# Performance work log

Hardware: AMD Instinct MI355X
Metric: run time of the kernel (lower is better)

## Reference

```python
import jax, jax.numpy as jnp
import numpy as np

DN = ('NCHW', 'OIHW', 'NCHW')

def _conv(x, w, b):
    y = jax.lax.conv_general_dilated(x, w, (2, 2), 'SAME', dimension_numbers=DN)
    return jax.nn.relu(y + b[None, :, None, None])

def setup_inputs() -> dict:
    key = jax.random.key(0)
    ks = jax.random.split(key, 20)
    B, S, V, D, NC = 64, 128, 32000, 512, 1000
    inp = {}
    inp['images'] = jax.random.normal(ks[0], (B, 3, 224, 224), jnp.float32)
    inp['sequences'] = jax.random.randint(ks[1], (B, S), 0, V)
    inp['lengths'] = jax.random.randint(ks[2], (B,), 1, S + 1)
    inp['lengths_var'] = inp['lengths']
    s = 0.02
    inp['emb'] = jax.random.normal(ks[3], (V, D), jnp.float32) * s
    # SimpleCNN(3): 4 strided conv blocks 3->64->128->256->512, final_dim=512
    chans = [3, 64, 128, 256, 512]
    for i in range(4):
        inp[f'cw{i+1}'] = jax.random.normal(ks[4 + i], (chans[i + 1], chans[i], 3, 3), jnp.float32) * s
        inp[f'cb{i+1}'] = jnp.zeros((chans[i + 1],), jnp.float32)
    inp['rnn_w'] = jax.random.normal(ks[8], (D, D), jnp.float32) * s
    inp['rnn_b'] = jnp.zeros((D,), jnp.float32)
    inp['fc1_w'] = jax.random.normal(ks[9], (D + 512, 512), jnp.float32) * s
    inp['fc1_b'] = jnp.zeros((512,), jnp.float32)
    inp['fc2_w'] = jax.random.normal(ks[10], (512, 512), jnp.float32) * s
    inp['fc2_b'] = jnp.zeros((512,), jnp.float32)
    inp['clf_w'] = jax.random.normal(ks[11], (512, NC), jnp.float32) * s
    inp['clf_b'] = jnp.zeros((NC,), jnp.float32)
    return inp

def reference(images, sequences, lengths, lengths_var, emb, cw1, cb1, cw2, cb2, cw3, cb3, cw4, cb4, rnn_w, rnn_b, fc1_w, fc1_b, fc2_w, fc2_b, clf_w, clf_b):
    B, S = sequences.shape
    # masked mean over valid tokens (replaces the per-sample python loop)
    we = emb[sequences]                                   # [B,S,512]
    mask = (jnp.arange(S)[None, :] < lengths[:, None]).astype(we.dtype)
    batch_means = (we * mask[:, :, None]).sum(1) / lengths.astype(we.dtype)[:, None]
    sent = batch_means @ rnn_w + rnn_b                    # [B,512]
    # SimpleCNN + global avg pool -> [B,512,1,1] -> squeeze
    x = _conv(images, cw1, cb1)
    x = _conv(x, cw2, cb2)
    x = _conv(x, cw3, cb3)
    x = _conv(x, cw4, cb4)
    img = x.mean(axis=(2, 3))                             # [B,512]
    feats = jnp.concatenate([img, sent], axis=1)          # [B,1024]
    h = jax.nn.relu(feats @ fc1_w + fc1_b)
    h = jax.nn.relu(h @ fc2_w + fc2_b)                    # dropout = identity (eval)
    return h @ clf_w + clf_b
```

## Files before the change

### kernel.cpp

```cpp
#include <hip/hip_runtime.h>
#include <hip/hip_bf16.h>
#include <cstddef>
#include <cstdint>

typedef unsigned short u16;
typedef __attribute__((ext_vector_type(8))) short bf16x8;
typedef __attribute__((ext_vector_type(4))) float f32x4;
typedef __attribute__((ext_vector_type(8))) unsigned short u16x8;

static __device__ __forceinline__ u16 f2bf(float x) {
  unsigned u = __float_as_uint(x);
  u += 0x7fffu + ((u >> 16) & 1u);
  return (u16)(u >> 16);
}
static __device__ __forceinline__ float bflo(unsigned u) { return __uint_as_float(u << 16); }
static __device__ __forceinline__ float bfhi(unsigned u) { return __uint_as_float(u & 0xffff0000u); }

static __device__ __forceinline__ void gll16(const u16* g, u16* l) {
  __builtin_amdgcn_global_load_lds(
      (const __attribute__((address_space(1))) void*)g,
      (__attribute__((address_space(3))) void*)l, 16, 0, 0);
}

static __device__ __forceinline__ int xcd_swizzle(int orig, int nwg) {
  const int q = nwg >> 3, r = nwg & 7;
  const int xcd = orig & 7, idx = orig >> 3;
  return (xcd < r ? xcd * (q + 1) : r * (q + 1) + (xcd - r) * q) + idx;
}


static __device__ __forceinline__ void halo_store_f(u16* buf, int IH, int PC,
                                                    int C, long long i) {
  const int c8n = C >> 3;
  const int c8 = (int)(i % c8n);
  long long rem = i / c8n;
  const int per = 2 * PC + 2 * IH;
  const int p = (int)(rem % per);
  const int n = (int)(rem / per);
  size_t row_off;
  if (p < 2 * PC) {
    row_off = ((size_t)(n * (IH + 1) + IH) * 2 * PC) + p;
  } else {
    const int q = p - 2 * PC;
    row_off = ((size_t)(n * (IH + 1) + (q >> 1)) * 2 * PC) + (q & 1) * PC + (PC - 1);
  }
  const u16x8 z = {0, 0, 0, 0, 0, 0, 0, 0};
  *(u16x8*)(buf + row_off * C + c8 * 8) = z;
}
__global__ __launch_bounds__(256) void zero_halo3(u16* __restrict__ A,
                                                  u16* __restrict__ B,
                                                  u16* __restrict__ Cb, int nimg) {
  long long i = (long long)blockIdx.x * 256 + threadIdx.x;
  const long long cA = (long long)nimg * 8 * (2 * 57 + 2 * 112);
  const long long cB = (long long)nimg * 16 * (2 * 29 + 2 * 56);
  const long long cC = (long long)nimg * 32 * (2 * 15 + 2 * 28);
  if (i < cA) { halo_store_f(A, 112, 57, 64, i); return; }
  i -= cA;
  if (i < cB) { halo_store_f(B, 56, 29, 128, i); return; }
  i -= cB;
  if (i < cC) halo_store_f(Cb, 28, 15, 256, i);
}

__global__ __launch_bounds__(256) void conv1_s2(
    const float* __restrict__ in,
    const float* __restrict__ w,
    const float* __restrict__ bias,
    u16* __restrict__ out) {
  __shared__ float sw[64 * 27];
  __shared__ float sb[64];
  __shared__ u16 so[256 * 64];
  const int tid = threadIdx.x;
  if (tid < 64) sb[tid] = bias[tid];
  for (int i = tid; i < 64 * 27; i += 256) sw[i] = w[i];
  __syncthreads();
  const int n = blockIdx.y;
  const int by = blockIdx.x / 7, bx = blockIdx.x % 7;
  const int oy = by * 16 + (tid >> 4), ox = bx * 16 + (tid & 15);
  const bool colv = (ox != 111);
  const float* ib = in + (size_t)n * 3 * 224 * 224 + (size_t)(2 * oy) * 224 + 2 * ox;

  float v[27];
  #pragma unroll
  for (int c = 0; c < 3; ++c)
    #pragma unroll
    for (int r = 0; r < 3; ++r) {
      const bool rowv = !(oy == 111 && r == 2);
      const float* rp = ib + (size_t)c * 50176 + r * 224;
      float2 p = {0.f, 0.f};
      float x2 = 0.f;
      if (rowv) {
        p = *(const float2*)rp;
        if (colv) x2 = rp[2];
      }
      v[c * 9 + r * 3 + 0] = p.x;
      v[c * 9 + r * 3 + 1] = p.y;
      v[c * 9 + r * 3 + 2] = x2;
    }

  #pragma unroll
  for (int kc = 0; kc < 8; ++kc) {
    u16x8 pack;
    #pragma unroll
    for (int k8 = 0; k8 < 8; ++k8) {
      const int k = kc * 8 + k8;
      float a = sb[k];
      const float* wk = &sw[k * 27];
      #pragma unroll
      for (int t = 0; t < 27; ++t) a = fmaf(v[t], wk[t], a);
      pack[k8] = f2bf(fmaxf(a, 0.f));
    }
    *(u16x8*)&so[(tid * 8 + (kc ^ (tid & 7))) * 8] = pack;
  }
  __syncthreads();
  #pragma unroll
  for (int it = 0; it < 8; ++it) {
    const int row = it * 2 + (tid >> 7);
    const int q = tid & 127;
    const int px = q >> 3, c8 = q & 7;
    const int p = row * 16 + px;
    u16x8 v8 = *(const u16x8*)&so[(p * 8 + (c8 ^ (p & 7))) * 8];
    const size_t ro = ((size_t)(n * 113 + by * 16 + row) * 2 + (px & 1)) * 57
                      + bx * 8 + (px >> 1);
    *(u16x8*)(out + ro * 64 + c8 * 8) = v8;
  }
}

static __device__ __forceinline__ void pack_one(const float* __restrict__ w,
                                                u16* __restrict__ pw,
                                                int CB, int NB, int C, int idx) {
  const int j = idx & 7;
  const int L = (idx >> 3) & 63;
  int t = idx >> 9;
  const int nbg = t % NB; t /= NB;
  const int cb = t % CB;
  const int tap = t / CB;
  const int n = nbg * 16 + (L & 15);
  const int c = cb * 32 + ((L >> 4) << 3) + j;
  pw[idx] = f2bf(w[((size_t)n * C + c) * 9 + tap]);
}
__global__ __launch_bounds__(256) void pack_all(
    const float* __restrict__ w2, const float* __restrict__ w3,
    const float* __restrict__ w4, u16* __restrict__ p2,
    u16* __restrict__ p3, u16* __restrict__ p4) {
  int i = blockIdx.x * 256 + threadIdx.x;
  if (i < 9 * 64 * 128) { pack_one(w2, p2, 2, 8, 64, i); return; }
  i -= 9 * 64 * 128;
  if (i < 9 * 128 * 256) { pack_one(w3, p3, 4, 16, 128, i); return; }
  i -= 9 * 128 * 256;
  if (i < 9 * 256 * 512) pack_one(w4, p4, 8, 32, 256, i);
}

template<int C, int K, int OH, int OW, bool OUT_FOLD>
__global__ __launch_bounds__(256, 3) void conv3x3s2_mfma(
    const u16* __restrict__ in,
    const u16* __restrict__ pw,
    const float* __restrict__ bias,
    u16* __restrict__ out,
    int M_total) {
  constexpr int IH = 2 * OH;
  constexpr int IPC = OW + 1;
  constexpr int IROW = 2 * IPC;
  constexpr int P = OH * OW;
  constexpr int CB = C / 32, NB = K / 16;
  constexpr int STEPS = 9 * CB;
  static_assert(STEPS % 3 == 0, "triple-buffer rotation needs STEPS%3==0");
  constexpr int OPC = OW / 2 + 1;

  __shared__ u16 lds[3][8192];

  const int bm = xcd_swizzle(blockIdx.x, gridDim.x);
  const int nbh = blockIdx.y;
  const int lane = threadIdx.x & 63, wv = threadIdx.x >> 6;
  const int mh = wv >> 1, nh = wv & 1;

  int s_aoff[4];
  #pragma unroll
  for (int mf = 0; mf < 4; ++mf) {
    int pm = bm * 128 + mh * 64 + mf * 16 + (lane & 15);
    if (pm >= M_total) pm = M_total - 1;
    const int n = pm / P;
    const int p = pm - n * P;
    const int oy = p / OW, ox = p - oy * OW;
    s_aoff[mf] = ((n * (IH + 1) + 2 * oy) * IROW + ox) * C + ((lane >> 4) << 3);
  }

  f32x4 acc[4][4];
  #pragma unroll
  for (int mf = 0; mf < 4; ++mf)
    #pragma unroll
    for (int nf = 0; nf < 4; ++nf) acc[mf][nf] = (f32x4){0.f, 0.f, 0.f, 0.f};

  auto STAGE = [&](int st, int buf) {
    if (nh == 0) {
      const int cb = st & (CB - 1);
      const int tap = st / CB;
      const int r = tap / 3, s = tap - 3 * r;
      const int toff = (r * IROW + (s & 1) * IPC + (s >> 1)) * C + cb * 32;
      #pragma unroll
      for (int mf = 0; mf < 4; ++mf)
        gll16(in + s_aoff[mf] + toff, &lds[buf][(mh * 4 + mf) * 512]);
    } else {
      const u16* bp = pw + ((size_t)st * NB + nbh * 8 + mh * 4) * 512 + lane * 8;
      #pragma unroll
      for (int nf = 0; nf < 4; ++nf)
        gll16(bp + nf * 512, &lds[buf][4096 + (mh * 4 + nf) * 512]);
    }
  };
  auto COMPUTE = [&](int buf) {
    bf16x8 a[4], b[4];
    #pragma unroll
    for (int mf = 0; mf < 4; ++mf)
      a[mf] = *(const bf16x8*)&lds[buf][(mh * 4 + mf) * 512 + lane * 8];
    #pragma unroll
    for (int nf = 0; nf < 4; ++nf)
      b[nf] = *(const bf16x8*)&lds[buf][4096 + (nh * 4 + nf) * 512 + lane * 8];
    #pragma unroll
    for (int mf = 0; mf < 4; ++mf)
      #pragma unroll
      for (int nf = 0; nf < 4; ++nf)
        acc[mf][nf] = __builtin_amdgcn_mfma_f32_16x16x32_bf16(a[mf], b[nf], acc[mf][nf], 0, 0, 0);
  };
  auto PHASE = [&](int s, int bufC, int bufS) {
    const bool more = (s + 2) < STEPS;
    if (more) STAGE(s + 2, bufS);
    __builtin_amdgcn_s_setprio(1);
    COMPUTE(bufC);
    __builtin_amdgcn_s_setprio(0);
    if (more) asm volatile("s_waitcnt vmcnt(4)" ::: "memory");
    else      asm volatile("s_waitcnt vmcnt(0)" ::: "memory");
    __builtin_amdgcn_s_barrier();
    __builtin_amdgcn_sched_barrier(0);
  };

  STAGE(0, 0);
  STAGE(1, 1);
  asm volatile("s_waitcnt vmcnt(4)" ::: "memory");
  __builtin_amdgcn_s_barrier();
  __builtin_amdgcn_sched_barrier(0);

  for (int st = 0; st < STEPS; st += 3) {
    PHASE(st + 0, 0, 2);
    PHASE(st + 1, 1, 0);
    PHASE(st + 2, 2, 1);
  }

  const int rowg = (lane >> 4) << 2;
  #pragma unroll
  for (int mf = 0; mf < 4; ++mf)
    #pragma unroll
    for (int nf = 0; nf < 4; ++nf) {
      const int ch = (nbh * 8 + nh * 4 + nf) * 16 + (lane & 15);
      const float bv = bias[ch];
      #pragma unroll
      for (int rr = 0; rr < 4; ++rr) {
        const int pm = bm * 128 + mh * 64 + mf * 16 + rowg + rr;
        if (pm < M_total) {
          const int n = pm / P;
          const int p = pm - n * P;
          const int oy = p / OW, ox = p - oy * OW;
          size_t ro;
          if (OUT_FOLD)
            ro = ((size_t)(n * (OH + 1) + oy) * 2 + (ox & 1)) * OPC + (ox >> 1);
          else
            ro = (size_t)(n * (OH + 1) + oy) * (OW + 1) + ox;
          out[ro * K + ch] = f2bf(fmaxf(acc[mf][nf][rr] + bv, 0.f));
        }
      }
    }
}

__global__ __launch_bounds__(256) void avgpool_nhwc(
    const u16* __restrict__ in, float* __restrict__ feats, int n0) {
  const int n = blockIdx.x, t = threadIdx.x;
  const u16* p = in + (size_t)n * (15 * 15 * 512) + t * 2;
  float s0 = 0.f, s1 = 0.f;
  for (int y = 0; y < 14; ++y)
    #pragma unroll
    for (int x = 0; x < 14; ++x) {
      unsigned u = *(const unsigned*)(p + (size_t)(y * 15 + x) * 512);
      s0 += bflo(u);
      s1 += bfhi(u);
    }
  float* f = feats + (size_t)(n0 + n) * 1024;
  f[2 * t] = s0 * (1.f / 196.f);
  f[2 * t + 1] = s1 * (1.f / 196.f);
}

__global__ __launch_bounds__(256) void embed_mean_kernel(
    const int* __restrict__ seq, const int* __restrict__ len,
    const float* __restrict__ emb, float* __restrict__ means) {
  __shared__ float part[3][512];
  const int b = blockIdx.x;
  const int L = len[b];
  const int sg = threadIdx.x >> 6;
  const int d0 = (threadIdx.x & 63) * 8;
  float a[8] = {0.f, 0.f, 0.f, 0.f, 0.f, 0.f, 0.f, 0.f};
  for (int s = sg; s < L; s += 4) {
    const float* e = emb + (size_t)seq[b * 128 + s] * 512 + d0;
    float4 v0 = *(const float4*)e, v1 = *(const float4*)(e + 4);
    a[0] += v0.x; a[1] += v0.y; a[2] += v0.z; a[3] += v0.w;
    a[4] += v1.x; a[5] += v1.y; a[6] += v1.z; a[7] += v1.w;
  }
  if (sg) {
    #pragma unroll
    for (int j = 0; j < 8; ++j) part[sg - 1][d0 + j] = a[j];
  }
  __syncthreads();
  if (sg == 0) {
    const float inv = 1.f / (float)L;
    #pragma unroll
    for (int j = 0; j < 8; ++j)
      means[(size_t)b * 512 + d0 + j] =
          (a[j] + part[0][d0 + j] + part[1][d0 + j] + part[2][d0 + j]) * inv;
  }
}

template<int K, int N, bool RELU>
__global__ __launch_bounds__(256) void fc_kernel(
    const float* __restrict__ x, int ldx,
    const float* __restrict__ w, const float* __restrict__ bias,
    float* __restrict__ out, int ldo) {
  __shared__ float row[2][K];
  const int m0 = blockIdx.y * 2;
  for (int i = threadIdx.x; i < 2 * K; i += 256)
    row[i / K][i % K] = x[(size_t)(m0 + i / K) * ldx + (i % K)];
  __syncthreads();
  const int col = blockIdx.x * 256 + threadIdx.x;
  if (col < N) {
    float acc[2][4] = {{0.f, 0.f, 0.f, 0.f}, {0.f, 0.f, 0.f, 0.f}};
    for (int k = 0; k < K; k += 4) {
      float w0 = w[(size_t)(k + 0) * N + col];
      float w1 = w[(size_t)(k + 1) * N + col];
      float w2 = w[(size_t)(k + 2) * N + col];
      float w3 = w[(size_t)(k + 3) * N + col];
      #pragma unroll
      for (int m = 0; m < 2; ++m) {
        acc[m][0] = fmaf(row[m][k + 0], w0, acc[m][0]);
        acc[m][1] = fmaf(row[m][k + 1], w1, acc[m][1]);
        acc[m][2] = fmaf(row[m][k + 2], w2, acc[m][2]);
        acc[m][3] = fmaf(row[m][k + 3], w3, acc[m][3]);
      }
    }
    const float bv = bias[col];
    #pragma unroll
    for (int m = 0; m < 2; ++m) {
      float a = acc[m][0] + acc[m][1] + acc[m][2] + acc[m][3] + bv;
      out[(size_t)(m0 + m) * ldo + col] = RELU ? fmaxf(a, 0.f) : a;
    }
  }
}

extern "C" void kernel_launch(void* const* d_in, const int* in_sizes, int n_in,
                              void* d_out, int out_size, void* d_ws, size_t ws_size,
                              hipStream_t stream) {
  const float* images = (const float*)d_in[0];
  const int*   seq    = (const int*)d_in[1];
  const int*   len    = (const int*)d_in[2];
  const float* emb    = (const float*)d_in[4];
  const float* cw1 = (const float*)d_in[5];  const float* cb1 = (const float*)d_in[6];
  const float* cw2 = (const float*)d_in[7];  const float* cb2 = (const float*)d_in[8];
  const float* cw3 = (const float*)d_in[9];  const float* cb3 = (const float*)d_in[10];
  const float* cw4 = (const float*)d_in[11]; const float* cb4 = (const float*)d_in[12];
  const float* rnn_w = (const float*)d_in[13]; const float* rnn_b = (const float*)d_in[14];
  const float* fc1_w = (const float*)d_in[15]; const float* fc1_b = (const float*)d_in[16];
  const float* fc2_w = (const float*)d_in[17]; const float* fc2_b = (const float*)d_in[18];
  const float* clf_w = (const float*)d_in[19]; const float* clf_b = (const float*)d_in[20];
  float* out = (float*)d_out;

  const size_t A_E = (size_t)113 * 2 * 57 * 64;
  const size_t B_E = (size_t)57 * 2 * 29 * 128;
  const size_t C_E = (size_t)29 * 2 * 15 * 256;
  const size_t D_E = (size_t)15 * 15 * 512;
  const size_t PW2_E = 9 * 64 * 128, PW3_E = 9 * 128 * 256, PW4_E = 9 * 256 * 512;
  const size_t PER_IMG = (A_E + B_E + C_E + D_E) * 2;
  const size_t FIXED = (PW2_E + PW3_E + PW4_E) * 2 +
                       (size_t)(64 * 512 + 64 * 1024 + 64 * 512 + 64 * 512) * 4;
  int chunk = 64;
  if (ws_size < FIXED + 64 * PER_IMG) {
    size_t avail = (ws_size > FIXED) ? (ws_size - FIXED) : 0;
    size_t c = avail / PER_IMG;
    chunk = (c < 1) ? 1 : (c > 64 ? 64 : (int)c);
  }
  u16* bufA = (u16*)d_ws;
  u16* bufB = bufA + (size_t)chunk * A_E;
  u16* bufC = bufB + (size_t)chunk * B_E;
  u16* bufD = bufC + (size_t)chunk * C_E;
  u16* pw2 = bufD + (size_t)chunk * D_E;
  u16* pw3 = pw2 + PW2_E;
  u16* pw4 = pw3 + PW3_E;
  float* means = (float*)(pw4 + PW4_E);
  float* feats = means + 64 * 512;
  float* h1 = feats + 64 * 1024;
  float* h2 = h1 + 64 * 512;

  {
    const int pk_total = 9 * 64 * 128 + 9 * 128 * 256 + 9 * 256 * 512;
    pack_all<<<(pk_total + 255) / 256, 256, 0, stream>>>(cw2, cw3, cw4, pw2, pw3, pw4);
    long long zt = (long long)chunk *
        (8 * (2 * 57 + 2 * 112) + 16 * (2 * 29 + 2 * 56) + 32 * (2 * 15 + 2 * 28));
    zero_halo3<<<(int)((zt + 255) / 256), 256, 0, stream>>>(bufA, bufB, bufC, chunk);
  }

  embed_mean_kernel<<<64, 256, 0, stream>>>(seq, len, emb, means);
  fc_kernel<512, 512, false><<<dim3(2, 32), 256, 0, stream>>>(
      means, 512, rnn_w, rnn_b, feats + 512, 1024);

  for (int n0 = 0; n0 < 64; n0 += chunk) {
    int nb = 64 - n0; if (nb > chunk) nb = chunk;
    conv1_s2<<<dim3(49, nb), 256, 0, stream>>>(
        images + (size_t)n0 * 3 * 224 * 224, cw1, cb1, bufA);
    const int M2 = nb * 56 * 56, M3 = nb * 28 * 28, M4 = nb * 14 * 14;
    conv3x3s2_mfma<64, 128, 56, 56, true><<<dim3((M2 + 127) / 128, 1), 256, 0, stream>>>(
        bufA, pw2, cb2, bufB, M2);
    conv3x3s2_mfma<128, 256, 28, 28, true><<<dim3((M3 + 127) / 128, 2), 256, 0, stream>>>(
        bufB, pw3, cb3, bufC, M3);
    conv3x3s2_mfma<256, 512, 14, 14, false><<<dim3((M4 + 127) / 128, 4), 256, 0, stream>>>(
        bufC, pw4, cb4, bufD, M4);
    avgpool_nhwc<<<nb, 256, 0, stream>>>(bufD, feats, n0);
  }

  fc_kernel<1024, 512, true ><<<dim3(2, 32), 256, 0, stream>>>(feats, 1024, fc1_w, fc1_b, h1, 512);
  fc_kernel<512,  512, true ><<<dim3(2, 32), 256, 0, stream>>>(h1,    512,  fc2_w, fc2_b, h2, 512);
  fc_kernel<512, 1000, false><<<dim3(4, 32), 256, 0, stream>>>(h2,    512,  clf_w, clf_b, out, 1000);
}
```

Before: 381.5 us.

## Run first conv layer on bf16 MFMA and split avgpool across four thread groups

Replaces the scalar FP32 FMA first convolution with an MFMA-based version. Each lane gathers its 27 input taps, padded to 32, converts them to bf16 and multiplies against a 64-channel weight matrix pre-packed in the pack kernel. This removes the heavy per-thread 27x64 FMA loop, at the cost of bf16 rounding of the image inputs and uncoalesced gathers. The avgpool kernel now uses 1024 threads, splitting the 196 spatial positions into four groups reduced through shared memory, to raise parallelism over only 64 blocks.

After: 385.7 us. Within noise of the previous version (+1.1%).

```diff
diff --git a/kernel.cpp b/kernel.cpp
--- a/kernel.cpp
+++ b/kernel.cpp
@@ -27,7 +27,6 @@
   const int xcd = orig & 7, idx = orig >> 3;
   return (xcd < r ? xcd * (q + 1) : r * (q + 1) + (xcd - r) * q) + idx;
 }
-
 
 static __device__ __forceinline__ void halo_store_f(u16* buf, int IH, int PC,
                                                     int C, long long i) {
@@ -61,67 +60,92 @@
   if (i < cC) halo_store_f(Cb, 28, 15, 256, i);
 }
 
-__global__ __launch_bounds__(256) void conv1_s2(
+__global__ __launch_bounds__(256) void conv1_mfma(
     const float* __restrict__ in,
-    const float* __restrict__ w,
+    const u16* __restrict__ pw1,
     const float* __restrict__ bias,
     u16* __restrict__ out) {
-  __shared__ float sw[64 * 27];
-  __shared__ float sb[64];
   __shared__ u16 so[256 * 64];
   const int tid = threadIdx.x;
-  if (tid < 64) sb[tid] = bias[tid];
-  for (int i = tid; i < 64 * 27; i += 256) sw[i] = w[i];
+  const int bm = blockIdx.x;
+  const int lane = tid & 63, wv = tid >> 6;
+  const int kq = lane >> 4;
+
+  bf16x8 b[4];
+  #pragma unroll
+  for (int nf = 0; nf < 4; ++nf)
+    b[nf] = *(const bf16x8*)(pw1 + ((size_t)(nf * 64 + lane)) * 8);
+
+#define LD1(c, r, s) \
+  ((((r) == 2) && yb) || (((s) == 2) && xb)) ? 0.f \
+      : bp[(c) * 50176 + (r) * 224 + (s)]
+
+  bf16x8 a[4];
+  #pragma unroll
+  for (int mf = 0; mf < 4; ++mf) {
+    const int pm = bm * 256 + wv * 64 + mf * 16 + (lane & 15);
+    const int n = pm / 12544, p = pm - n * 12544;
+    const int oy = p / 112, ox = p - oy * 112;
+    const bool yb = (oy == 111), xb = (ox == 111);
+    const float* bp = in + (size_t)n * 150528 + (size_t)(2 * oy) * 224 + 2 * ox;
+    float v[8];
+    if (kq == 0) {
+      v[0] = LD1(0, 0, 0); v[1] = LD1(0, 0, 1); v[2] = LD1(0, 0, 2);
+      v[3] = LD1(0, 1, 0); v[4] = LD1(0, 1, 1); v[5] = LD1(0, 1, 2);
+      v[6] = LD1(0, 2, 0); v[7] = LD1(0, 2, 1);
+    } else if (kq == 1) {
+      v[0] = LD1(0, 2, 2); v[1] = LD1(1, 0, 0); v[2] = LD1(1, 0, 1);
+      v[3] = LD1(1, 0, 2); v[4] = LD1(1, 1, 0); v[5] = LD1(1, 1, 1);
+      v[6] = LD1(1, 1, 2); v[7] = LD1(1, 2, 0);
+    } else if (kq == 2) {
+      v[0] = LD1(1, 2, 1); v[1] = LD1(1, 2, 2); v[2] = LD1(2, 0, 0);
+      v[3] = LD1(2, 0, 1); v[4] = LD1(2, 0, 2); v[5] = LD1(2, 1, 0);
+      v[6] = LD1(2, 1, 1); v[7] = LD1(2, 1, 2);
+    } else {
+      v[0] = LD1(2, 2, 0); v[1] = LD1(2, 2, 1); v[2] = LD1(2, 2, 2);
+      v[3] = 0.f; v[4] = 0.f; v[5] = 0.f; v[6] = 0.f; v[7] = 0.f;
+    }
+    #pragma unroll
+    for (int j = 0; j < 8; ++j) a[mf][j] = (short)f2bf(v[j]);
+  }
+#undef LD1
+
+  f32x4 acc[4][4];
+  #pragma unroll
+  for (int mf = 0; mf < 4; ++mf)
+    #pragma unroll
+    for (int nf = 0; nf < 4; ++nf) {
+      acc[mf][nf] = (f32x4){0.f, 0.f, 0.f, 0.f};
+      acc[mf][nf] = __builtin_amdgcn_mfma_f32_16x16x32_bf16(a[mf], b[nf], acc[mf][nf], 0, 0, 0);
+    }
+
+  const int rowg = (lane >> 4) << 2;
+  #pragma unroll
+  for (int nf = 0; nf < 4; ++nf) {
+    const int ch = nf * 16 + (lane & 15);
+    const float bv = bias[ch];
+    const int c8 = ch >> 3, cj = ch & 7;
+    #pragma unroll
+    for (int mf = 0; mf < 4; ++mf)
+      #pragma unroll
+      for (int rr = 0; rr < 4; ++rr) {
+        const int pl = wv * 64 + mf * 16 + rowg + rr;
+        so[(pl * 8 + (c8 ^ (pl & 7))) * 8 + cj] =
+            f2bf(fmaxf(acc[mf][nf][rr] + bv, 0.f));
+      }
+  }
   __syncthreads();
-  const int n = blockIdx.y;
-  const int by = blockIdx.x / 7, bx = blockIdx.x % 7;
-  const int oy = by * 16 + (tid >> 4), ox = bx * 16 + (tid & 15);
-  const bool colv = (ox != 111);
-  const float* ib = in + (size_t)n * 3 * 224 * 224 + (size_t)(2 * oy) * 224 + 2 * ox;
-
-  float v[27];
-  #pragma unroll
-  for (int c = 0; c < 3; ++c)
-    #pragma unroll
-    for (int r = 0; r < 3; ++r) {
-      const bool rowv = !(oy == 111 && r == 2);
-      const float* rp = ib + (size_t)c * 50176 + r * 224;
-      float2 p = {0.f, 0.f};
-      float x2 = 0.f;
-      if (rowv) {
-        p = *(const float2*)rp;
-        if (colv) x2 = rp[2];
-      }
-      v[c * 9 + r * 3 + 0] = p.x;
-      v[c * 9 + r * 3 + 1] = p.y;
-      v[c * 9 + r * 3 + 2] = x2;
-    }
-
-  #pragma unroll
-  for (int kc = 0; kc < 8; ++kc) {
-    u16x8 pack;
-    #pragma unroll
-    for (int k8 = 0; k8 < 8; ++k8) {
-      const int k = kc * 8 + k8;
-      float a = sb[k];
-      const float* wk = &sw[k * 27];
-      #pragma unroll
-      for (int t = 0; t < 27; ++t) a = fmaf(v[t], wk[t], a);
-      pack[k8] = f2bf(fmaxf(a, 0.f));
-    }
-    *(u16x8*)&so[(tid * 8 + (kc ^ (tid & 7))) * 8] = pack;
-  }
-  __syncthreads();
+
+  const int nimg = bm / 49, pb = (bm % 49) * 256;
   #pragma unroll
   for (int it = 0; it < 8; ++it) {
-    const int row = it * 2 + (tid >> 7);
-    const int q = tid & 127;
-    const int px = q >> 3, c8 = q & 7;
-    const int p = row * 16 + px;
-    u16x8 v8 = *(const u16x8*)&so[(p * 8 + (c8 ^ (p & 7))) * 8];
-    const size_t ro = ((size_t)(n * 113 + by * 16 + row) * 2 + (px & 1)) * 57
-                      + bx * 8 + (px >> 1);
-    *(u16x8*)(out + ro * 64 + c8 * 8) = v8;
+    const int q = it * 256 + tid;
+    const int pl = q >> 3, c8 = q & 7;
+    u16x8 vv = *(const u16x8*)&so[(pl * 8 + (c8 ^ (pl & 7))) * 8];
+    const int p = pb + pl;
+    const int oy = p / 112, ox = p - oy * 112;
+    const size_t ro = ((size_t)(nimg * 113 + oy) * 2 + (ox & 1)) * 57 + (ox >> 1);
+    *(u16x8*)(out + ro * 64 + c8 * 8) = vv;
   }
 }
 
@@ -139,10 +163,19 @@
   pw[idx] = f2bf(w[((size_t)n * C + c) * 9 + tap]);
 }
 __global__ __launch_bounds__(256) void pack_all(
-    const float* __restrict__ w2, const float* __restrict__ w3,
-    const float* __restrict__ w4, u16* __restrict__ p2,
+    const float* __restrict__ w1, const float* __restrict__ w2,
+    const float* __restrict__ w3, const float* __restrict__ w4,
+    u16* __restrict__ p1, u16* __restrict__ p2,
     u16* __restrict__ p3, u16* __restrict__ p4) {
   int i = blockIdx.x * 256 + threadIdx.x;
+  if (i < 2048) {
+    const int j = i & 7, L = (i >> 3) & 63, nf = i >> 9;
+    const int n = nf * 16 + (L & 15);
+    const int k = ((L >> 4) << 3) + j;
+    p1[i] = (k < 27) ? f2bf(w1[n * 27 + k]) : (u16)0;
+    return;
+  }
+  i -= 2048;
   if (i < 9 * 64 * 128) { pack_one(w2, p2, 2, 8, 64, i); return; }
   i -= 9 * 64 * 128;
   if (i < 9 * 128 * 256) { pack_one(w3, p3, 4, 16, 128, i); return; }
@@ -269,21 +302,28 @@
     }
 }
 
-__global__ __launch_bounds__(256) void avgpool_nhwc(
+__global__ __launch_bounds__(1024) void avgpool_nhwc(
     const u16* __restrict__ in, float* __restrict__ feats, int n0) {
-  const int n = blockIdx.x, t = threadIdx.x;
-  const u16* p = in + (size_t)n * (15 * 15 * 512) + t * 2;
+  __shared__ float part[3][512];
+  const int n = blockIdx.x;
+  const int g = threadIdx.x >> 8, i = threadIdx.x & 255;
+  const u16* p = in + (size_t)n * (15 * 15 * 512) + i * 2;
   float s0 = 0.f, s1 = 0.f;
-  for (int y = 0; y < 14; ++y)
-    #pragma unroll
-    for (int x = 0; x < 14; ++x) {
-      unsigned u = *(const unsigned*)(p + (size_t)(y * 15 + x) * 512);
-      s0 += bflo(u);
-      s1 += bfhi(u);
-    }
-  float* f = feats + (size_t)(n0 + n) * 1024;
-  f[2 * t] = s0 * (1.f / 196.f);
-  f[2 * t + 1] = s1 * (1.f / 196.f);
+  for (int q = g * 49; q < g * 49 + 49; ++q) {
+    const int y = q / 14, x = q - y * 14;
+    unsigned u = *(const unsigned*)(p + (size_t)(y * 15 + x) * 512);
+    s0 += bflo(u);
+    s1 += bfhi(u);
+  }
+  if (g) { part[g - 1][2 * i] = s0; part[g - 1][2 * i + 1] = s1; }
+  __syncthreads();
+  if (g == 0) {
+    s0 += part[0][2 * i] + part[1][2 * i] + part[2][2 * i];
+    s1 += part[0][2 * i + 1] + part[1][2 * i + 1] + part[2][2 * i + 1];
+    float* f = feats + (size_t)(n0 + n) * 1024;
+    f[2 * i] = s0 * (1.f / 196.f);
+    f[2 * i + 1] = s1 * (1.f / 196.f);
+  }
 }
 
 __global__ __launch_bounds__(256) void embed_mean_kernel(
@@ -371,9 +411,10 @@
   const size_t B_E = (size_t)57 * 2 * 29 * 128;
   const size_t C_E = (size_t)29 * 2 * 15 * 256;
   const size_t D_E = (size_t)15 * 15 * 512;
+  const size_t PW1_E = 2048;
   const size_t PW2_E = 9 * 64 * 128, PW3_E = 9 * 128 * 256, PW4_E = 9 * 256 * 512;
   const size_t PER_IMG = (A_E + B_E + C_E + D_E) * 2;
-  const size_t FIXED = (PW2_E + PW3_E + PW4_E) * 2 +
+  const size_t FIXED = (PW1_E + PW2_E + PW3_E + PW4_E) * 2 +
                        (size_t)(64 * 512 + 64 * 1024 + 64 * 512 + 64 * 512) * 4;
   int chunk = 64;
   if (ws_size < FIXED + 64 * PER_IMG) {
@@ -385,7 +426,8 @@
   u16* bufB = bufA + (size_t)chunk * A_E;
   u16* bufC = bufB + (size_t)chunk * B_E;
   u16* bufD = bufC + (size_t)chunk * C_E;
-  u16* pw2 = bufD + (size_t)chunk * D_E;
+  u16* pw1 = bufD + (size_t)chunk * D_E;
+  u16* pw2 = pw1 + PW1_E;
   u16* pw3 = pw2 + PW2_E;
   u16* pw4 = pw3 + PW3_E;
   float* means = (float*)(pw4 + PW4_E);
@@ -394,8 +436,9 @@
   float* h2 = h1 + 64 * 512;
 
   {
-    const int pk_total = 9 * 64 * 128 + 9 * 128 * 256 + 9 * 256 * 512;
-    pack_all<<<(pk_total + 255) / 256, 256, 0, stream>>>(cw2, cw3, cw4, pw2, pw3, pw4);
+    const int pk_total = 2048 + 9 * 64 * 128 + 9 * 128 * 256 + 9 * 256 * 512;
+    pack_all<<<(pk_total + 255) / 256, 256, 0, stream>>>(
+        cw1, cw2, cw3, cw4, pw1, pw2, pw3, pw4);
     long long zt = (long long)chunk *
         (8 * (2 * 57 + 2 * 112) + 16 * (2 * 29 + 2 * 56) + 32 * (2 * 15 + 2 * 28));
     zero_halo3<<<(int)((zt + 255) / 256), 256, 0, stream>>>(bufA, bufB, bufC, chunk);
@@ -407,8 +450,8 @@
 
   for (int n0 = 0; n0 < 64; n0 += chunk) {
     int nb = 64 - n0; if (nb > chunk) nb = chunk;
-    conv1_s2<<<dim3(49, nb), 256, 0, stream>>>(
-        images + (size_t)n0 * 3 * 224 * 224, cw1, cb1, bufA);
+    conv1_mfma<<<dim3(nb * 49), 256, 0, stream>>>(
+        images + (size_t)n0 * 150528, pw1, cb1, bufA);
     const int M2 = nb * 56 * 56, M3 = nb * 28 * 28, M4 = nb * 14 * 14;
     conv3x3s2_mfma<64, 128, 56, 56, true><<<dim3((M2 + 127) / 128, 1), 256, 0, stream>>>(
         bufA, pw2, cb2, bufB, M2);
@@ -416,7 +459,7 @@
         bufB, pw3, cb3, bufC, M3);
     conv3x3s2_mfma<256, 512, 14, 14, false><<<dim3((M4 + 127) / 128, 4), 256, 0, stream>>>(
         bufC, pw4, cb4, bufD, M4);
-    avgpool_nhwc<<<nb, 256, 0, stream>>>(bufD, feats, n0);
+    avgpool_nhwc<<<nb, 1024, 0, stream>>>(bufD, feats, n0);
   }
 
   fc_kernel<1024, 512, true ><<<dim3(2, 32), 256, 0, stream>>>(feats, 1024, fc1_w, fc1_b, h1, 512);
```
